# Optimization experiments

Hardware: AMD Instinct MI355X
Metric: run time of the kernel (lower is better)

## Reference

```python
import jax, jax.numpy as jnp
import numpy as np

B, S, H = 2, 1024, 1024
N_IN, N_PROC = 512, 32


def _l2norm(x, eps=1e-12):
    n = jnp.linalg.norm(x, axis=-1, keepdims=True)
    return x / jnp.maximum(n, eps)


def setup_inputs() -> dict:
    key = jax.random.key(0)
    k1, k2, k3, k4 = jax.random.split(key, 4)
    intermediate = jax.random.normal(k1, (B, S, H), dtype=jnp.float32)
    input_activations = jax.random.normal(k2, (B, S, N_IN), dtype=jnp.float32)
    # params (torch defaults: pattern_templates ~ randn; Linear weight ~ U scaled)
    pattern_templates = jax.random.normal(k3, (N_PROC, N_IN), dtype=jnp.float32)
    bound = 1.0 / np.sqrt(H)
    W_transform = jax.random.uniform(k4, (N_PROC * H, H), dtype=jnp.float32,
                                     minval=-bound, maxval=bound)
    return {"intermediate": intermediate, "input_activations": input_activations,
            "pattern_templates": pattern_templates, "W_transform": W_transform}


def reference(intermediate, input_activations, pattern_templates, W_transform):
    # pattern matching -> soft routing weights  [B,S,N_proc]
    act_norm = _l2norm(input_activations)
    tmpl_norm = _l2norm(pattern_templates)
    process_activations = jax.nn.sigmoid(
        jnp.einsum('bsi,ni->bsn', act_norm, tmpl_norm))
    # dispatch: weighted sum over sequence (batched GEMM instead of bcast-mul-sum)
    contexts = jnp.einsum('bsh,bsn->bnh', intermediate, process_activations)
    norm = process_activations.sum(axis=1)[..., None] + 1e-8  # [B,N_proc,1]
    contexts = contexts / norm
    # per-process-neuron HxH transform (torch Linear weight is [out,in])
    Wn = W_transform.reshape(N_PROC, H, H)  # [n, k(out), h(in)]
    transformed = jnp.einsum('bnh,nkh->bnk', contexts, Wn)
    # combine back to tokens  [B,S,H]
    combined = jnp.einsum('bnh,bsn->bsh', transformed, process_activations)
    return combined, process_activations
```

## Files before the change

kernel.cpp:

```cpp
#include <hip/hip_runtime.h>
#include <math.h>

#define B 2
#define S 1024
#define H 1024
#define NIN 512
#define NP 32
#define SC 16
#define SCHUNK (S / SC)

__global__ __launch_bounds__(256)
void k_pattern(const float* __restrict__ act, const float* __restrict__ tmpl,
               float* __restrict__ P, float* __restrict__ nrm) {
    __shared__ float act_lds[8][NIN];
    __shared__ float invn[NP];
    __shared__ float psum[8][NP];
    int tid = threadIdx.x;
    int t0 = blockIdx.x * 8;
    int b  = t0 >> 10;

    {
        const float4* src = (const float4*)(act + (size_t)t0 * NIN);
        float4* dst = (float4*)(&act_lds[0][0]);
        for (int k = tid; k < 8 * NIN / 4; k += 256) dst[k] = src[k];
    }
    {
        int n = tid >> 3, s8 = tid & 7;
        const float* tr = tmpl + (size_t)n * NIN;
        float ss = 0.f;
#pragma unroll 16
        for (int k = 0; k < 64; ++k) { float x = tr[s8 + 8 * k]; ss += x * x; }
        ss += __shfl_xor(ss, 1); ss += __shfl_xor(ss, 2); ss += __shfl_xor(ss, 4);
        if (s8 == 0) invn[n] = 1.f / fmaxf(sqrtf(ss), 1e-12f);
    }
    __syncthreads();

    int tok = tid >> 5;
    int sub = tid & 31;
    float ss = 0.f;
#pragma unroll
    for (int k = 0; k < 16; ++k) { float x = act_lds[tok][sub + 32 * k]; ss += x * x; }
#pragma unroll
    for (int m = 16; m; m >>= 1) ss += __shfl_xor(ss, m);
    float inva = 1.f / fmaxf(sqrtf(ss), 1e-12f);

    float4 av[4];
#pragma unroll
    for (int q = 0; q < 4; ++q)
        av[q] = *(const float4*)(&act_lds[tok][sub * 4 + q * 128]);

    float dot[NP];
#pragma unroll
    for (int n = 0; n < NP; ++n) {
        const float* tr = tmpl + (size_t)n * NIN + sub * 4;
        float d = 0.f;
#pragma unroll
        for (int q = 0; q < 4; ++q) {
            float4 tv = *(const float4*)(tr + q * 128);
            d += tv.x * av[q].x + tv.y * av[q].y + tv.z * av[q].z + tv.w * av[q].w;
        }
        dot[n] = d;
    }
    float myd = 0.f;
#pragma unroll
    for (int n = 0; n < NP; ++n) {
        float d = dot[n];
        d += __shfl_xor(d, 1); d += __shfl_xor(d, 2); d += __shfl_xor(d, 4);
        d += __shfl_xor(d, 8); d += __shfl_xor(d, 16);
        if (sub == n) myd = d;
    }
    float p = 1.f / (1.f + expf(-myd * inva * invn[sub]));
    P[(size_t)(t0 + tok) * NP + sub] = p;
    psum[tok][sub] = p;
    __syncthreads();
    if (tid < NP) {
        float s = 0.f;
#pragma unroll
        for (int t = 0; t < 8; ++t) s += psum[t][tid];
        unsafeAtomicAdd(&nrm[b * NP + tid], s);
    }
}

__global__ __launch_bounds__(256)
void k_ctx_partial(const float* __restrict__ I, const float* __restrict__ P,
                   float* __restrict__ part) {
    int bid = blockIdx.x;
    int ht = bid & 7;
    int sc = (bid >> 3) & (SC - 1);
    int b  = bid >> 7;
    int tid = threadIdx.x;
    int hl = tid & 127;
    int g  = __builtin_amdgcn_readfirstlane(tid >> 7);
    int h  = ht * 128 + hl;
    int s0 = sc * SCHUNK;
    const float* Pb = P + ((size_t)b * S + s0) * NP + g * 16;
    const float* Ip = I + ((size_t)b * S + s0) * H + h;
    float acc[16];
#pragma unroll
    for (int j = 0; j < 16; ++j) acc[j] = 0.f;
#pragma unroll 4
    for (int s = 0; s < SCHUNK; ++s) {
        float x = Ip[(size_t)s * H];
#pragma unroll
        for (int j = 0; j < 16; ++j) acc[j] += x * Pb[s * NP + j];
    }
    size_t base = (((size_t)b * SC + sc) * NP + g * 16) * H + h;
#pragma unroll
    for (int j = 0; j < 16; ++j) part[base + (size_t)j * H] = acc[j];
}

__global__ __launch_bounds__(256)
void k_ctx_reduce(const float* __restrict__ part, float* __restrict__ ctx) {
    int idx = blockIdx.x * 256 + threadIdx.x;
    int b = idx >> 15;
    int rem = idx & 32767;
    float s = 0.f;
#pragma unroll
    for (int sc = 0; sc < SC; ++sc)
        s += part[((size_t)b * SC + sc) * (NP * H) + rem];
    ctx[idx] = s;
}

__global__ __launch_bounds__(256, 4)
void k_transform(const float* __restrict__ W, const float* __restrict__ ctx,
                 const float* __restrict__ nrm, float* __restrict__ T) {
    int bid = blockIdx.x;
    int n  = bid >> 6;
    int rg = bid & 63;
    int tid = threadIdx.x;
    int w = tid >> 6, lane = tid & 63;

    float inv0 = 1.f / (nrm[n] + 1e-8f);
    float inv1 = 1.f / (nrm[NP + n] + 1e-8f);

    const float4* c0g = (const float4*)(ctx + (size_t)n * H);
    const float4* c1g = (const float4*)(ctx + ((size_t)NP + n) * H);
    float4 c0[4], c1[4];
#pragma unroll
    for (int it = 0; it < 4; ++it) {
        float4 v = c0g[it * 64 + lane];
        c0[it] = make_float4(v.x * inv0, v.y * inv0, v.z * inv0, v.w * inv0);
        float4 u = c1g[it * 64 + lane];
        c1[it] = make_float4(u.x * inv1, u.y * inv1, u.z * inv1, u.w * inv1);
    }

    int row0 = rg * 16 + w * 4;
    const float4* Wr = (const float4*)(W + ((size_t)n * H + row0) * H);
    float a0[4] = {0.f, 0.f, 0.f, 0.f};
    float a1[4] = {0.f, 0.f, 0.f, 0.f};
#pragma unroll
    for (int it = 0; it < 4; ++it) {
#pragma unroll
        for (int r = 0; r < 4; ++r) {
            float4 wv = Wr[r * 256 + it * 64 + lane];
            a0[r] += wv.x * c0[it].x + wv.y * c0[it].y + wv.z * c0[it].z + wv.w * c0[it].w;
            a1[r] += wv.x * c1[it].x + wv.y * c1[it].y + wv.z * c1[it].z + wv.w * c1[it].w;
        }
    }
#pragma unroll
    for (int r = 0; r < 4; ++r) {
#pragma unroll
        for (int off = 32; off; off >>= 1) {
            a0[r] += __shfl_xor(a0[r], off);
            a1[r] += __shfl_xor(a1[r], off);
        }
    }
    if (lane == 0) {
#pragma unroll
        for (int r = 0; r < 4; ++r) {
            T[(size_t)n * H + row0 + r] = a0[r];
            T[((size_t)NP + n) * H + row0 + r] = a1[r];
        }
    }
}

__global__ __launch_bounds__(256)
void k_combine(const float* __restrict__ T, const float* __restrict__ P,
               float* __restrict__ out) {
    int bid = blockIdx.x;
    int ht = bid & 3;
    int sc = (bid >> 2) & 63;
    int b  = bid >> 8;
    int tid = threadIdx.x;
    __shared__ float Tl[NP][256];
    int h0 = ht * 256;
    for (int k = tid; k < NP * 256; k += 256) {
        int n = k >> 8, h = k & 255;
        Tl[n][h] = T[((size_t)b * NP + n) * H + h0 + h];
    }
    __syncthreads();
    int s0 = sc * 16;
    const float* Pb = P + ((size_t)b * S + s0) * NP;
    float acc[16];
#pragma unroll
    for (int s = 0; s < 16; ++s) acc[s] = 0.f;
#pragma unroll
    for (int n0 = 0; n0 < NP; n0 += 4) {
        float t0v = Tl[n0 + 0][tid];
        float t1v = Tl[n0 + 1][tid];
        float t2v = Tl[n0 + 2][tid];
        float t3v = Tl[n0 + 3][tid];
#pragma unroll
        for (int s = 0; s < 16; ++s) {
            const float* pr = Pb + s * NP + n0;
            acc[s] += t0v * pr[0] + t1v * pr[1] + t2v * pr[2] + t3v * pr[3];
        }
    }
#pragma unroll
    for (int s = 0; s < 16; ++s)
        out[((size_t)b * S + s0 + s) * H + h0 + tid] = acc[s];
}

extern "C" void kernel_launch(void* const* d_in, const int* in_sizes, int n_in,
                              void* d_out, int out_size, void* d_ws, size_t ws_size,
                              hipStream_t stream) {
    const float* I    = (const float*)d_in[0];
    const float* act  = (const float*)d_in[1];
    const float* tmpl = (const float*)d_in[2];
    const float* W    = (const float*)d_in[3];
    float* out  = (float*)d_out;
    float* Pout = out + (size_t)B * S * H;

    float* ws   = (float*)d_ws;
    float* nrm  = ws;
    float* part = nrm + 64;
    float* ctx  = part + (size_t)B * SC * NP * H;
    float* T    = ctx + (size_t)B * NP * H;

    hipMemsetAsync(nrm, 0, (size_t)B * NP * sizeof(float), stream);
    k_pattern    <<<B * S / 8,            256, 0, stream>>>(act, tmpl, Pout, nrm);
    k_ctx_partial<<<B * SC * 8,           256, 0, stream>>>(I, Pout, part);
    k_ctx_reduce <<<B * NP * H / 256,     256, 0, stream>>>(part, ctx);
    k_transform  <<<NP * 64,              256, 0, stream>>>(W, ctx, nrm, T);
    k_combine    <<<B * 64 * 4,           256, 0, stream>>>(T, Pout, out);
}
```

Measured before the change: 81.37 us.

## Retile context partial GEMM, stage context in LDS, halve rows per transform block

After: 75.04 us. 1.08x faster.

```diff
diff --git a/kernel.cpp b/kernel.cpp
--- a/kernel.cpp
+++ b/kernel.cpp
@@ -6,8 +6,11 @@
 #define H 1024
 #define NIN 512
 #define NP 32
-#define SC 16
-#define SCHUNK (S / SC)
+#define SC2 32
+
+__device__ __forceinline__ float dot4(float4 a, float4 b) {
+    return a.x * b.x + a.y * b.y + a.z * b.z + a.w * b.w;
+}
 
 __global__ __launch_bounds__(256)
 void k_pattern(const float* __restrict__ act, const float* __restrict__ tmpl,
@@ -35,36 +38,26 @@
     }
     __syncthreads();
 
-    int tok = tid >> 5;
-    int sub = tid & 31;
+    int tok = tid >> 5, sub = tid & 31;
+    const float* arow = &act_lds[tok][0];
     float ss = 0.f;
 #pragma unroll
-    for (int k = 0; k < 16; ++k) { float x = act_lds[tok][sub + 32 * k]; ss += x * x; }
+    for (int k = 0; k < 16; ++k) { float x = arow[sub + 32 * k]; ss += x * x; }
 #pragma unroll
     for (int m = 16; m; m >>= 1) ss += __shfl_xor(ss, m);
     float inva = 1.f / fmaxf(sqrtf(ss), 1e-12f);
 
     float4 av[4];
 #pragma unroll
-    for (int q = 0; q < 4; ++q)
-        av[q] = *(const float4*)(&act_lds[tok][sub * 4 + q * 128]);
-
-    float dot[NP];
+    for (int q = 0; q < 4; ++q) av[q] = *(const float4*)(arow + sub * 4 + q * 128);
+
+    float myd = 0.f;
 #pragma unroll
     for (int n = 0; n < NP; ++n) {
-        const float* tr = tmpl + (size_t)n * NIN + sub * 4;
+        const float* trp = tmpl + (size_t)n * NIN + sub * 4;
         float d = 0.f;
 #pragma unroll
-        for (int q = 0; q < 4; ++q) {
-            float4 tv = *(const float4*)(tr + q * 128);
-            d += tv.x * av[q].x + tv.y * av[q].y + tv.z * av[q].z + tv.w * av[q].w;
-        }
-        dot[n] = d;
-    }
-    float myd = 0.f;
-#pragma unroll
-    for (int n = 0; n < NP; ++n) {
-        float d = dot[n];
+        for (int q = 0; q < 4; ++q) d += dot4(*(const float4*)(trp + q * 128), av[q]);
         d += __shfl_xor(d, 1); d += __shfl_xor(d, 2); d += __shfl_xor(d, 4);
         d += __shfl_xor(d, 8); d += __shfl_xor(d, 16);
         if (sub == n) myd = d;
@@ -84,109 +77,111 @@
 __global__ __launch_bounds__(256)
 void k_ctx_partial(const float* __restrict__ I, const float* __restrict__ P,
                    float* __restrict__ part) {
+    __shared__ float4 Pl4[SC2 * NP / 4];
     int bid = blockIdx.x;
-    int ht = bid & 7;
-    int sc = (bid >> 3) & (SC - 1);
-    int b  = bid >> 7;
-    int tid = threadIdx.x;
-    int hl = tid & 127;
-    int g  = __builtin_amdgcn_readfirstlane(tid >> 7);
-    int h  = ht * 128 + hl;
-    int s0 = sc * SCHUNK;
-    const float* Pb = P + ((size_t)b * S + s0) * NP + g * 16;
-    const float* Ip = I + ((size_t)b * S + s0) * H + h;
-    float acc[16];
-#pragma unroll
-    for (int j = 0; j < 16; ++j) acc[j] = 0.f;
+    int sc = bid & 31, ht = (bid >> 5) & 3, b = bid >> 7;
+    int tid = threadIdx.x;
+    int s0 = sc * 32;
+    Pl4[tid] = ((const float4*)(P + ((size_t)b * S + s0) * NP))[tid];
+    __syncthreads();
+
+    int hq = tid & 63, ng = tid >> 6;
+    int h = ht * 256 + hq * 4;
+    const float4* I4 = (const float4*)(I) + ((size_t)b * S + s0) * (H / 4) + (h >> 2);
+    float4 acc[8];
+#pragma unroll
+    for (int j = 0; j < 8; ++j) acc[j] = make_float4(0.f, 0.f, 0.f, 0.f);
 #pragma unroll 4
-    for (int s = 0; s < SCHUNK; ++s) {
-        float x = Ip[(size_t)s * H];
-#pragma unroll
-        for (int j = 0; j < 16; ++j) acc[j] += x * Pb[s * NP + j];
-    }
-    size_t base = (((size_t)b * SC + sc) * NP + g * 16) * H + h;
-#pragma unroll
-    for (int j = 0; j < 16; ++j) part[base + (size_t)j * H] = acc[j];
+    for (int s = 0; s < 32; ++s) {
+        float4 iv = I4[s * (H / 4)];
+        float4 pa = Pl4[s * 8 + ng * 2];
+        float4 pb = Pl4[s * 8 + ng * 2 + 1];
+        acc[0].x += iv.x * pa.x; acc[0].y += iv.y * pa.x; acc[0].z += iv.z * pa.x; acc[0].w += iv.w * pa.x;
+        acc[1].x += iv.x * pa.y; acc[1].y += iv.y * pa.y; acc[1].z += iv.z * pa.y; acc[1].w += iv.w * pa.y;
+        acc[2].x += iv.x * pa.z; acc[2].y += iv.y * pa.z; acc[2].z += iv.z * pa.z; acc[2].w += iv.w * pa.z;
+        acc[3].x += iv.x * pa.w; acc[3].y += iv.y * pa.w; acc[3].z += iv.z * pa.w; acc[3].w += iv.w * pa.w;
+        acc[4].x += iv.x * pb.x; acc[4].y += iv.y * pb.x; acc[4].z += iv.z * pb.x; acc[4].w += iv.w * pb.x;
+        acc[5].x += iv.x * pb.y; acc[5].y += iv.y * pb.y; acc[5].z += iv.z * pb.y; acc[5].w += iv.w * pb.y;
+        acc[6].x += iv.x * pb.z; acc[6].y += iv.y * pb.z; acc[6].z += iv.z * pb.z; acc[6].w += iv.w * pb.z;
+        acc[7].x += iv.x * pb.w; acc[7].y += iv.y * pb.w; acc[7].z += iv.z * pb.w; acc[7].w += iv.w * pb.w;
+    }
+    int n0 = ng * 8;
+    size_t base = ((size_t)(b * SC2 + sc) * NP + n0) * H + h;
+#pragma unroll
+    for (int j = 0; j < 8; ++j)
+        *(float4*)(part + base + (size_t)j * H) = acc[j];
 }
 
 __global__ __launch_bounds__(256)
 void k_ctx_reduce(const float* __restrict__ part, float* __restrict__ ctx) {
     int idx = blockIdx.x * 256 + threadIdx.x;
-    int b = idx >> 15;
-    int rem = idx & 32767;
+    int b = idx >> 15, rem = idx & 32767;
     float s = 0.f;
 #pragma unroll
-    for (int sc = 0; sc < SC; ++sc)
-        s += part[((size_t)b * SC + sc) * (NP * H) + rem];
+    for (int sc = 0; sc < SC2; ++sc)
+        s += part[((size_t)b * SC2 + sc) * (NP * H) + rem];
     ctx[idx] = s;
 }
 
-__global__ __launch_bounds__(256, 4)
+__global__ __launch_bounds__(256)
 void k_transform(const float* __restrict__ W, const float* __restrict__ ctx,
                  const float* __restrict__ nrm, float* __restrict__ T) {
+    __shared__ float4 cl4[512];
     int bid = blockIdx.x;
-    int n  = bid >> 6;
-    int rg = bid & 63;
-    int tid = threadIdx.x;
-    int w = tid >> 6, lane = tid & 63;
-
+    int n = bid >> 7, rg = bid & 127;
+    int tid = threadIdx.x;
     float inv0 = 1.f / (nrm[n] + 1e-8f);
     float inv1 = 1.f / (nrm[NP + n] + 1e-8f);
-
-    const float4* c0g = (const float4*)(ctx + (size_t)n * H);
-    const float4* c1g = (const float4*)(ctx + ((size_t)NP + n) * H);
-    float4 c0[4], c1[4];
+    {
+        float4 v = ((const float4*)(ctx + (size_t)n * H))[tid];
+        cl4[tid] = make_float4(v.x * inv0, v.y * inv0, v.z * inv0, v.w * inv0);
+        float4 u = ((const float4*)(ctx + ((size_t)NP + n) * H))[tid];
+        cl4[256 + tid] = make_float4(u.x * inv1, u.y * inv1, u.z * inv1, u.w * inv1);
+    }
+    __syncthreads();
+
+    int w = tid >> 6, lane = tid & 63;
+    int r0 = rg * 8 + w * 2;
+    const float4* W0 = (const float4*)(W + ((size_t)n * H + r0) * H);
+    const float4* W1 = W0 + (H / 4);
+    float a00 = 0.f, a01 = 0.f, a10 = 0.f, a11 = 0.f;
 #pragma unroll
     for (int it = 0; it < 4; ++it) {
-        float4 v = c0g[it * 64 + lane];
-        c0[it] = make_float4(v.x * inv0, v.y * inv0, v.z * inv0, v.w * inv0);
-        float4 u = c1g[it * 64 + lane];
-        c1[it] = make_float4(u.x * inv1, u.y * inv1, u.z * inv1, u.w * inv1);
-    }
-
-    int row0 = rg * 16 + w * 4;
-    const float4* Wr = (const float4*)(W + ((size_t)n * H + row0) * H);
-    float a0[4] = {0.f, 0.f, 0.f, 0.f};
-    float a1[4] = {0.f, 0.f, 0.f, 0.f};
-#pragma unroll
-    for (int it = 0; it < 4; ++it) {
-#pragma unroll
-        for (int r = 0; r < 4; ++r) {
-            float4 wv = Wr[r * 256 + it * 64 + lane];
-            a0[r] += wv.x * c0[it].x + wv.y * c0[it].y + wv.z * c0[it].z + wv.w * c0[it].w;
-            a1[r] += wv.x * c1[it].x + wv.y * c1[it].y + wv.z * c1[it].z + wv.w * c1[it].w;
-        }
-    }
-#pragma unroll
-    for (int r = 0; r < 4; ++r) {
-#pragma unroll
-        for (int off = 32; off; off >>= 1) {
-            a0[r] += __shfl_xor(a0[r], off);
-            a1[r] += __shfl_xor(a1[r], off);
-        }
+        int ix = it * 64 + lane;
+        float4 f0 = cl4[ix];
+        float4 f1 = cl4[256 + ix];
+        float4 w0 = W0[ix];
+        float4 w1 = W1[ix];
+        a00 += dot4(w0, f0); a01 += dot4(w0, f1);
+        a10 += dot4(w1, f0); a11 += dot4(w1, f1);
+    }
+#pragma unroll
+    for (int off = 32; off; off >>= 1) {
+        a00 += __shfl_xor(a00, off); a01 += __shfl_xor(a01, off);
+        a10 += __shfl_xor(a10, off); a11 += __shfl_xor(a11, off);
     }
     if (lane == 0) {
-#pragma unroll
-        for (int r = 0; r < 4; ++r) {
-            T[(size_t)n * H + row0 + r] = a0[r];
-            T[((size_t)NP + n) * H + row0 + r] = a1[r];
-        }
+        T[(size_t)n * H + r0] = a00;
+        T[((size_t)NP + n) * H + r0] = a01;
+        T[(size_t)n * H + r0 + 1] = a10;
+        T[((size_t)NP + n) * H + r0 + 1] = a11;
     }
 }
 
 __global__ __launch_bounds__(256)
 void k_combine(const float* __restrict__ T, const float* __restrict__ P,
                float* __restrict__ out) {
+    __shared__ float Tl[NP][256];
     int bid = blockIdx.x;
-    int ht = bid & 3;
-    int sc = (bid >> 2) & 63;
-    int b  = bid >> 8;
-    int tid = threadIdx.x;
-    __shared__ float Tl[NP][256];
+    int ht = bid & 3, sc = (bid >> 2) & 63, b = bid >> 8;
+    int tid = threadIdx.x;
     int h0 = ht * 256;
-    for (int k = tid; k < NP * 256; k += 256) {
-        int n = k >> 8, h = k & 255;
-        Tl[n][h] = T[((size_t)b * NP + n) * H + h0 + h];
+    {
+        float4* dst = (float4*)(&Tl[0][0]);
+        for (int k = tid; k < NP * 64; k += 256) {
+            int n = k >> 6, hq = k & 63;
+            dst[k] = *(const float4*)(T + ((size_t)b * NP + n) * H + h0 + hq * 4);
+        }
     }
     __syncthreads();
     int s0 = sc * 16;
@@ -224,13 +219,13 @@
     float* ws   = (float*)d_ws;
     float* nrm  = ws;
     float* part = nrm + 64;
-    float* ctx  = part + (size_t)B * SC * NP * H;
+    float* ctx  = part + (size_t)B * SC2 * NP * H;
     float* T    = ctx + (size_t)B * NP * H;
 
     hipMemsetAsync(nrm, 0, (size_t)B * NP * sizeof(float), stream);
-    k_pattern    <<<B * S / 8,            256, 0, stream>>>(act, tmpl, Pout, nrm);
-    k_ctx_partial<<<B * SC * 8,           256, 0, stream>>>(I, Pout, part);
-    k_ctx_reduce <<<B * NP * H / 256,     256, 0, stream>>>(part, ctx);
-    k_transform  <<<NP * 64,              256, 0, stream>>>(W, ctx, nrm, T);
-    k_combine    <<<B * 64 * 4,           256, 0, stream>>>(T, Pout, out);
-}
+    k_pattern    <<<B * S / 8,        256, 0, stream>>>(act, tmpl, Pout, nrm);
+    k_ctx_partial<<<B * 4 * SC2,      256, 0, stream>>>(I, Pout, part);
+    k_ctx_reduce <<<B * NP * H / 256, 256, 0, stream>>>(part, ctx);
+    k_transform  <<<NP * 128,         256, 0, stream>>>(W, ctx, nrm, T);
+    k_combine    <<<B * 64 * 4,       256, 0, stream>>>(T, Pout, out);
+}
```
